# Optimization experiments

Measured on AMD Instinct MI355X. Metric: run time of the kernel, lower is better.

## Reference

```python
import jax, jax.numpy as jnp
import numpy as np


def _procrustes_align(X, Y):
    """Batched similarity-transform (scipy-style Procrustes, reflection allowed).
    Aligns Y (pred) to X (target). X, Y: [B, N, 3]. Returns aligned Y: [B, N, 3].
    """
    muX = X.mean(axis=1, keepdims=True)                      # [B,1,3]
    muY = Y.mean(axis=1, keepdims=True)
    X0 = X - muX
    Y0 = Y - muY
    normX = jnp.sqrt((X0 ** 2).sum(axis=(1, 2), keepdims=True))  # [B,1,1]
    normY = jnp.sqrt((Y0 ** 2).sum(axis=(1, 2), keepdims=True))
    X0n = X0 / normX
    Y0n = Y0 / normY
    # 3x3 cross-covariance per batch element
    M = jnp.einsum('bni,bnj->bij', X0n, Y0n)                 # [B,3,3]
    U, s, Vt = jnp.linalg.svd(M)                             # batched tiny SVD
    # Optimal rotation Q = V @ U^T = (U @ Vt)^T  (minimizes ||Y0n @ Q - X0n||)
    Q = jnp.swapaxes(jnp.matmul(U, Vt), -1, -2)              # [B,3,3]
    traceTA = s.sum(-1)[:, None, None]                       # [B,1,1]
    Z = normX * traceTA * jnp.einsum('bni,bij->bnj', Y0n, Q) + muX
    return Z


def setup_inputs() -> dict:
    key = jax.random.key(0)
    k1, k2 = jax.random.split(key)
    B, N = 262144, 21
    pred_kp3d = jax.random.normal(k1, (B, N, 3), dtype=jnp.float32)
    target_kp3d = jax.random.normal(k2, (B, N, 3), dtype=jnp.float32)
    return {"pred_kp3d": pred_kp3d, "target_kp3d": target_kp3d}


def reference(pred_kp3d, target_kp3d):
    pred_aligned = _procrustes_align(target_kp3d, pred_kp3d)
    # mean per-joint Euclidean distance (PA-MPJPE style)
    err = jnp.sqrt(((pred_aligned - target_kp3d) ** 2).sum(-1)).mean()
    return err
```

## Files before the change

### kernel.cpp

```cpp
#include <hip/hip_runtime.h>
#include <math.h>

#define NPTS 21
#define FLB  63
#define BPW  32
#define THREADS 64
#define TVEC (BPW * FLB / 4)
#define FULLR (TVEC / 64)
#define TAILL (TVEC % 64)
#define KMAX 11

__global__ __launch_bounds__(THREADS, 4)
void pa_mpjpe(const float* __restrict__ pred,
              const float* __restrict__ targ,
              float* __restrict__ ws,
              int B)
{
    __shared__ __align__(16) float ly[BPW * FLB];
    __shared__ __align__(16) float lx[BPW * FLB];

    const int lane = threadIdx.x & 63;
    const int b    = lane & (BPW - 1);
    const int sub  = (lane >> 5) & 1;
    const int b0   = blockIdx.x * BPW;

    const float4* gp = (const float4*)(pred + (size_t)b0 * FLB);
    const float4* gt = (const float4*)(targ + (size_t)b0 * FLB);
    float4 rp[FULLR + 1], rt[FULLR + 1];
    #pragma unroll
    for (int j = 0; j < FULLR; ++j) rp[j] = gp[j * 64 + lane];
    if (lane < TAILL)               rp[FULLR] = gp[FULLR * 64 + lane];
    #pragma unroll
    for (int j = 0; j < FULLR; ++j) rt[j] = gt[j * 64 + lane];
    if (lane < TAILL)               rt[FULLR] = gt[FULLR * 64 + lane];

    {
        float4* wy = (float4*)ly;
        float4* wx = (float4*)lx;
        #pragma unroll
        for (int j = 0; j < FULLR; ++j) wy[j * 64 + lane] = rp[j];
        if (lane < TAILL)               wy[FULLR * 64 + lane] = rp[FULLR];
        #pragma unroll
        for (int j = 0; j < FULLR; ++j) wx[j * 64 + lane] = rt[j];
        if (lane < TAILL)               wx[FULLR * 64 + lane] = rt[FULLR];
    }

    float py0[KMAX], py1[KMAX], py2[KMAX];
    float sy0=0.f, sy1=0.f, sy2=0.f, syy=0.f;
    float sx0=0.f, sx1=0.f, sx2=0.f;
    float m00=0,m01=0,m02=0, m10=0,m11=0,m12=0, m20=0,m21=0,m22=0;
    const int base = b * FLB;
    #pragma unroll
    for (int k = 0; k < KMAX; ++k) {
        const int n = 2 * k + sub;
        if (n < NPTS) {
            const int o = base + 3 * n;
            float a = ly[o+0], e = ly[o+1], c = ly[o+2];
            float u = lx[o+0], v = lx[o+1], x2 = lx[o+2];
            py0[k] = a; py1[k] = e; py2[k] = c;
            sy0 += a; sy1 += e; sy2 += c;
            syy = fmaf(a, a, fmaf(e, e, fmaf(c, c, syy)));
            sx0 += u; sx1 += v; sx2 += x2;
            m00 = fmaf(u,a,m00); m01 = fmaf(u,e,m01); m02 = fmaf(u,c,m02);
            m10 = fmaf(v,a,m10); m11 = fmaf(v,e,m11); m12 = fmaf(v,c,m12);
            m20 = fmaf(x2,a,m20); m21 = fmaf(x2,e,m21); m22 = fmaf(x2,c,m22);
        } else {
            py0[k] = 0.f; py1[k] = 0.f; py2[k] = 0.f;
        }
    }

    #define COMB(v) { v += __shfl_xor(v, 32, 64); }
    COMB(sy0) COMB(sy1) COMB(sy2) COMB(syy)
    COMB(sx0) COMB(sx1) COMB(sx2)
    COMB(m00) COMB(m01) COMB(m02)
    COMB(m10) COMB(m11) COMB(m12)
    COMB(m20) COMB(m21) COMB(m22)
    #undef COMB

    const float invN = 1.0f / (float)NPTS;
    float mux0 = sx0*invN, mux1 = sx1*invN, mux2 = sx2*invN;
    float muy0 = sy0*invN, muy1 = sy1*invN, muy2 = sy2*invN;
    float ny2  = syy - (sy0*sy0 + sy1*sy1 + sy2*sy2) * invN;
    float c00 = m00 - sx0*sy0*invN, c01 = m01 - sx0*sy1*invN, c02 = m02 - sx0*sy2*invN;
    float c10 = m10 - sx1*sy0*invN, c11 = m11 - sx1*sy1*invN, c12 = m12 - sx1*sy2*invN;
    float c20 = m20 - sx2*sy0*invN, c21 = m21 - sx2*sy1*invN, c22 = m22 - sx2*sy2*invN;

    float q00=c00, q01=c10, q02=c20,
          q10=c01, q11=c11, q12=c21,
          q20=c02, q21=c12, q22=c22;
    #pragma unroll
    for (int it = 0; it < 6; ++it) {
        float C00 = q11*q22 - q12*q21;
        float C01 = q12*q20 - q10*q22;
        float C02 = q10*q21 - q11*q20;
        float C10 = q02*q21 - q01*q22;
        float C11 = q00*q22 - q02*q20;
        float C12 = q01*q20 - q00*q21;
        float C20 = q01*q12 - q02*q11;
        float C21 = q02*q10 - q00*q12;
        float C22 = q00*q11 - q01*q10;
        float det = q00*C00 + q01*C01 + q02*C02;
        float ad  = fmaxf(fabsf(det), 1e-30f);
        float sdet = copysignf(ad, det);
        float g  = __expf(0.333333333f * __logf(ad));
        float ha = 0.5f / g;
        float hb = 0.5f * g / sdet;
        q00 = ha*q00 + hb*C00; q01 = ha*q01 + hb*C01; q02 = ha*q02 + hb*C02;
        q10 = ha*q10 + hb*C10; q11 = ha*q11 + hb*C11; q12 = ha*q12 + hb*C12;
        q20 = ha*q20 + hb*C20; q21 = ha*q21 + hb*C21; q22 = ha*q22 + hb*C22;
    }

    float trP = q00*c00 + q01*c10 + q02*c20
              + q10*c01 + q11*c11 + q12*c21
              + q20*c02 + q21*c12 + q22*c22;
    float kk = trP / ny2;
    float r00=kk*q00, r01=kk*q01, r02=kk*q02;
    float r10=kk*q10, r11=kk*q11, r12=kk*q12;
    float r20=kk*q20, r21=kk*q21, r22=kk*q22;

    float errsum = 0.0f;
    #pragma unroll
    for (int k = 0; k < KMAX; ++k) {
        const int n = 2 * k + sub;
        if (n < NPTS) {
            const int o = base + 3 * n;
            float xa = lx[o+0], xb = lx[o+1], xc = lx[o+2];
            float u = py0[k] - muy0, v = py1[k] - muy1, x2 = py2[k] - muy2;
            float z0 = fmaf(u, r00, fmaf(v, r10, fmaf(x2, r20, mux0))) - xa;
            float z1 = fmaf(u, r01, fmaf(v, r11, fmaf(x2, r21, mux1))) - xb;
            float z2 = fmaf(u, r02, fmaf(v, r12, fmaf(x2, r22, mux2))) - xc;
            errsum += sqrtf(fmaf(z0, z0, fmaf(z1, z1, z2*z2)));
        }
    }

    #pragma unroll
    for (int off = 32; off > 0; off >>= 1) errsum += __shfl_down(errsum, off, 64);
    if (lane == 0) ws[blockIdx.x] = errsum;
}

__global__ __launch_bounds__(256)
void pa_reduce(const float* __restrict__ ws, float* __restrict__ out,
               int nblk, float inv_total)
{
    __shared__ float sw[4];
    float s = 0.0f;
    const float4* w4 = (const float4*)ws;
    const int n4 = nblk >> 2;
    for (int i = threadIdx.x; i < n4; i += 256) {
        float4 v = w4[i];
        s += (v.x + v.y) + (v.z + v.w);
    }
    #pragma unroll
    for (int off = 32; off > 0; off >>= 1) s += __shfl_down(s, off, 64);
    if ((threadIdx.x & 63) == 0) sw[threadIdx.x >> 6] = s;
    __syncthreads();
    if (threadIdx.x == 0)
        out[0] = (sw[0] + sw[1] + sw[2] + sw[3]) * inv_total;
}

extern "C" void kernel_launch(void* const* d_in, const int* in_sizes, int n_in,
                              void* d_out, int out_size, void* d_ws, size_t ws_size,
                              hipStream_t stream)
{
    const float* pred = (const float*)d_in[0];
    const float* targ = (const float*)d_in[1];
    float* out = (float*)d_out;
    float* ws  = (float*)d_ws;

    int B = in_sizes[0] / FLB;
    int grid = (B + BPW - 1) / BPW;
    float inv_total = 1.0f / ((float)B * (float)NPTS);

    pa_mpjpe<<<grid, THREADS, 0, stream>>>(pred, targ, ws, B);
    pa_reduce<<<1, 256, 0, stream>>>(ws, out, grid, inv_total);
}
```

Measured before the change: 156.9 us.

## Process two batch chunks per block with a single reused LDS buffer and prefetch

Each 64-thread block now handles two 32-element chunks instead of one. A single LDS buffer is reused for pred then target, and the next chunk's global loads are issued while the current chunk is computed. Scheduling barriers fix the order so loads overlap compute. The goal is to hide global memory latency and halve LDS use per block, at the cost of more registers (occupancy hint lowered from 4 to 3) and half as many blocks.

```diff
diff --git a/kernel.cpp b/kernel.cpp
--- a/kernel.cpp
+++ b/kernel.cpp
@@ -3,135 +3,156 @@
 
 #define NPTS 21
 #define FLB  63
-#define BPW  32
+#define CB   32
+#define BPW  (2 * CB)
 #define THREADS 64
-#define TVEC (BPW * FLB / 4)
-#define FULLR (TVEC / 64)
-#define TAILL (TVEC % 64)
+#define TVEC (CB * FLB / 4)
+#define TAILL 56
 #define KMAX 11
 
-__global__ __launch_bounds__(THREADS, 4)
+#define SBAR() __builtin_amdgcn_sched_barrier(0)
+
+#define LOAD8(v, g) do { \
+    v##0 = (g)[0*64+lane]; v##1 = (g)[1*64+lane]; v##2 = (g)[2*64+lane]; \
+    v##3 = (g)[3*64+lane]; v##4 = (g)[4*64+lane]; v##5 = (g)[5*64+lane]; \
+    v##6 = (g)[6*64+lane]; if (lane < TAILL) v##7 = (g)[7*64+lane]; } while(0)
+
+#define STORE8(v) do { \
+    w4[0*64+lane] = v##0; w4[1*64+lane] = v##1; w4[2*64+lane] = v##2; \
+    w4[3*64+lane] = v##3; w4[4*64+lane] = v##4; w4[5*64+lane] = v##5; \
+    w4[6*64+lane] = v##6; if (lane < TAILL) w4[7*64+lane] = v##7; } while(0)
+
+#define PASSA() do { \
+    sy0=0.f; sy1=0.f; sy2=0.f; syy=0.f; \
+    _Pragma("unroll") \
+    for (int k = 0; k < KMAX; ++k) { \
+        const int n = 2*k + sub; \
+        if (n < NPTS) { \
+            const int o = base + 3*n; \
+            float a = sb[o+0], e = sb[o+1], c = sb[o+2]; \
+            py0[k]=a; py1[k]=e; py2[k]=c; \
+            sy0+=a; sy1+=e; sy2+=c; \
+            syy = fmaf(a,a,fmaf(e,e,fmaf(c,c,syy))); \
+        } else { py0[k]=0.f; py1[k]=0.f; py2[k]=0.f; } \
+    } } while(0)
+
+#define COMB(v) { v += __shfl_xor(v, 32, 64); }
+
+#define PASSB() do { \
+    float sx0=0.f, sx1=0.f, sx2=0.f; \
+    float m00=0,m01=0,m02=0, m10=0,m11=0,m12=0, m20=0,m21=0,m22=0; \
+    _Pragma("unroll") \
+    for (int k = 0; k < KMAX; ++k) { \
+        const int n = 2*k + sub; \
+        if (n < NPTS) { \
+            const int o = base + 3*n; \
+            float u = sb[o+0], v = sb[o+1], x2 = sb[o+2]; \
+            float a = py0[k], e = py1[k], c = py2[k]; \
+            sx0+=u; sx1+=v; sx2+=x2; \
+            m00=fmaf(u,a,m00); m01=fmaf(u,e,m01); m02=fmaf(u,c,m02); \
+            m10=fmaf(v,a,m10); m11=fmaf(v,e,m11); m12=fmaf(v,c,m12); \
+            m20=fmaf(x2,a,m20); m21=fmaf(x2,e,m21); m22=fmaf(x2,c,m22); \
+        } \
+    } \
+    COMB(sy0) COMB(sy1) COMB(sy2) COMB(syy) \
+    COMB(sx0) COMB(sx1) COMB(sx2) \
+    COMB(m00) COMB(m01) COMB(m02) \
+    COMB(m10) COMB(m11) COMB(m12) \
+    COMB(m20) COMB(m21) COMB(m22) \
+    const float invN = 1.0f / (float)NPTS; \
+    float mux0=sx0*invN, mux1=sx1*invN, mux2=sx2*invN; \
+    float muy0=sy0*invN, muy1=sy1*invN, muy2=sy2*invN; \
+    float ny2 = syy - (sy0*sy0 + sy1*sy1 + sy2*sy2) * invN; \
+    float c00=m00-sx0*sy0*invN, c01=m01-sx0*sy1*invN, c02=m02-sx0*sy2*invN; \
+    float c10=m10-sx1*sy0*invN, c11=m11-sx1*sy1*invN, c12=m12-sx1*sy2*invN; \
+    float c20=m20-sx2*sy0*invN, c21=m21-sx2*sy1*invN, c22=m22-sx2*sy2*invN; \
+    float q00=c00, q01=c10, q02=c20, \
+          q10=c01, q11=c11, q12=c21, \
+          q20=c02, q21=c12, q22=c22; \
+    _Pragma("unroll") \
+    for (int it = 0; it < 6; ++it) { \
+        float C00=q11*q22-q12*q21, C01=q12*q20-q10*q22, C02=q10*q21-q11*q20; \
+        float C10=q02*q21-q01*q22, C11=q00*q22-q02*q20, C12=q01*q20-q00*q21; \
+        float C20=q01*q12-q02*q11, C21=q02*q10-q00*q12, C22=q00*q11-q01*q10; \
+        float det = q00*C00 + q01*C01 + q02*C02; \
+        float ad  = fmaxf(fabsf(det), 1e-30f); \
+        float sdet = copysignf(ad, det); \
+        float g  = __expf(0.333333333f * __logf(ad)); \
+        float ha = 0.5f / g; \
+        float hb = 0.5f * g / sdet; \
+        q00=ha*q00+hb*C00; q01=ha*q01+hb*C01; q02=ha*q02+hb*C02; \
+        q10=ha*q10+hb*C10; q11=ha*q11+hb*C11; q12=ha*q12+hb*C12; \
+        q20=ha*q20+hb*C20; q21=ha*q21+hb*C21; q22=ha*q22+hb*C22; \
+    } \
+    float trP = q00*c00 + q01*c10 + q02*c20 \
+              + q10*c01 + q11*c11 + q12*c21 \
+              + q20*c02 + q21*c12 + q22*c22; \
+    float kk = trP / ny2; \
+    float r00=kk*q00, r01=kk*q01, r02=kk*q02; \
+    float r10=kk*q10, r11=kk*q11, r12=kk*q12; \
+    float r20=kk*q20, r21=kk*q21, r22=kk*q22; \
+    _Pragma("unroll") \
+    for (int k = 0; k < KMAX; ++k) { \
+        const int n = 2*k + sub; \
+        if (n < NPTS) { \
+            const int o = base + 3*n; \
+            float xa = sb[o+0], xb = sb[o+1], xc = sb[o+2]; \
+            float u = py0[k]-muy0, v = py1[k]-muy1, x2 = py2[k]-muy2; \
+            float z0 = fmaf(u,r00,fmaf(v,r10,fmaf(x2,r20,mux0))) - xa; \
+            float z1 = fmaf(u,r01,fmaf(v,r11,fmaf(x2,r21,mux1))) - xb; \
+            float z2 = fmaf(u,r02,fmaf(v,r12,fmaf(x2,r22,mux2))) - xc; \
+            errsum += sqrtf(fmaf(z0,z0,fmaf(z1,z1,z2*z2))); \
+        } \
+    } } while(0)
+
+__global__ __launch_bounds__(THREADS, 3)
 void pa_mpjpe(const float* __restrict__ pred,
               const float* __restrict__ targ,
               float* __restrict__ ws,
               int B)
 {
-    __shared__ __align__(16) float ly[BPW * FLB];
-    __shared__ __align__(16) float lx[BPW * FLB];
+    __shared__ __align__(16) float sb[CB * FLB];
+    float4* w4 = (float4*)sb;
 
     const int lane = threadIdx.x & 63;
-    const int b    = lane & (BPW - 1);
+    const int b    = lane & (CB - 1);
     const int sub  = (lane >> 5) & 1;
+    const int base = b * FLB;
     const int b0   = blockIdx.x * BPW;
 
-    const float4* gp = (const float4*)(pred + (size_t)b0 * FLB);
-    const float4* gt = (const float4*)(targ + (size_t)b0 * FLB);
-    float4 rp[FULLR + 1], rt[FULLR + 1];
-    #pragma unroll
-    for (int j = 0; j < FULLR; ++j) rp[j] = gp[j * 64 + lane];
-    if (lane < TAILL)               rp[FULLR] = gp[FULLR * 64 + lane];
-    #pragma unroll
-    for (int j = 0; j < FULLR; ++j) rt[j] = gt[j * 64 + lane];
-    if (lane < TAILL)               rt[FULLR] = gt[FULLR * 64 + lane];
+    const float4* gp0 = (const float4*)(pred + (size_t)b0 * FLB);
+    const float4* gt0 = (const float4*)(targ + (size_t)b0 * FLB);
+    const float4* gp1 = gp0 + TVEC;
+    const float4* gt1 = gt0 + TVEC;
 
-    {
-        float4* wy = (float4*)ly;
-        float4* wx = (float4*)lx;
-        #pragma unroll
-        for (int j = 0; j < FULLR; ++j) wy[j * 64 + lane] = rp[j];
-        if (lane < TAILL)               wy[FULLR * 64 + lane] = rp[FULLR];
-        #pragma unroll
-        for (int j = 0; j < FULLR; ++j) wx[j * 64 + lane] = rt[j];
-        if (lane < TAILL)               wx[FULLR * 64 + lane] = rt[FULLR];
-    }
+    float4 rp0, rp1, rp2, rp3, rp4, rp5, rp6, rp7 = make_float4(0,0,0,0);
+    float4 rt0, rt1, rt2, rt3, rt4, rt5, rt6, rt7 = make_float4(0,0,0,0);
+    float py0[KMAX], py1[KMAX], py2[KMAX];
+    float sy0, sy1, sy2, syy;
+    float errsum = 0.0f;
 
-    float py0[KMAX], py1[KMAX], py2[KMAX];
-    float sy0=0.f, sy1=0.f, sy2=0.f, syy=0.f;
-    float sx0=0.f, sx1=0.f, sx2=0.f;
-    float m00=0,m01=0,m02=0, m10=0,m11=0,m12=0, m20=0,m21=0,m22=0;
-    const int base = b * FLB;
-    #pragma unroll
-    for (int k = 0; k < KMAX; ++k) {
-        const int n = 2 * k + sub;
-        if (n < NPTS) {
-            const int o = base + 3 * n;
-            float a = ly[o+0], e = ly[o+1], c = ly[o+2];
-            float u = lx[o+0], v = lx[o+1], x2 = lx[o+2];
-            py0[k] = a; py1[k] = e; py2[k] = c;
-            sy0 += a; sy1 += e; sy2 += c;
-            syy = fmaf(a, a, fmaf(e, e, fmaf(c, c, syy)));
-            sx0 += u; sx1 += v; sx2 += x2;
-            m00 = fmaf(u,a,m00); m01 = fmaf(u,e,m01); m02 = fmaf(u,c,m02);
-            m10 = fmaf(v,a,m10); m11 = fmaf(v,e,m11); m12 = fmaf(v,c,m12);
-            m20 = fmaf(x2,a,m20); m21 = fmaf(x2,e,m21); m22 = fmaf(x2,c,m22);
-        } else {
-            py0[k] = 0.f; py1[k] = 0.f; py2[k] = 0.f;
-        }
-    }
-
-    #define COMB(v) { v += __shfl_xor(v, 32, 64); }
-    COMB(sy0) COMB(sy1) COMB(sy2) COMB(syy)
-    COMB(sx0) COMB(sx1) COMB(sx2)
-    COMB(m00) COMB(m01) COMB(m02)
-    COMB(m10) COMB(m11) COMB(m12)
-    COMB(m20) COMB(m21) COMB(m22)
-    #undef COMB
-
-    const float invN = 1.0f / (float)NPTS;
-    float mux0 = sx0*invN, mux1 = sx1*invN, mux2 = sx2*invN;
-    float muy0 = sy0*invN, muy1 = sy1*invN, muy2 = sy2*invN;
-    float ny2  = syy - (sy0*sy0 + sy1*sy1 + sy2*sy2) * invN;
-    float c00 = m00 - sx0*sy0*invN, c01 = m01 - sx0*sy1*invN, c02 = m02 - sx0*sy2*invN;
-    float c10 = m10 - sx1*sy0*invN, c11 = m11 - sx1*sy1*invN, c12 = m12 - sx1*sy2*invN;
-    float c20 = m20 - sx2*sy0*invN, c21 = m21 - sx2*sy1*invN, c22 = m22 - sx2*sy2*invN;
-
-    float q00=c00, q01=c10, q02=c20,
-          q10=c01, q11=c11, q12=c21,
-          q20=c02, q21=c12, q22=c22;
-    #pragma unroll
-    for (int it = 0; it < 6; ++it) {
-        float C00 = q11*q22 - q12*q21;
-        float C01 = q12*q20 - q10*q22;
-        float C02 = q10*q21 - q11*q20;
-        float C10 = q02*q21 - q01*q22;
-        float C11 = q00*q22 - q02*q20;
-        float C12 = q01*q20 - q00*q21;
-        float C20 = q01*q12 - q02*q11;
-        float C21 = q02*q10 - q00*q12;
-        float C22 = q00*q11 - q01*q10;
-        float det = q00*C00 + q01*C01 + q02*C02;
-        float ad  = fmaxf(fabsf(det), 1e-30f);
-        float sdet = copysignf(ad, det);
-        float g  = __expf(0.333333333f * __logf(ad));
-        float ha = 0.5f / g;
-        float hb = 0.5f * g / sdet;
-        q00 = ha*q00 + hb*C00; q01 = ha*q01 + hb*C01; q02 = ha*q02 + hb*C02;
-        q10 = ha*q10 + hb*C10; q11 = ha*q11 + hb*C11; q12 = ha*q12 + hb*C12;
-        q20 = ha*q20 + hb*C20; q21 = ha*q21 + hb*C21; q22 = ha*q22 + hb*C22;
-    }
-
-    float trP = q00*c00 + q01*c10 + q02*c20
-              + q10*c01 + q11*c11 + q12*c21
-              + q20*c02 + q21*c12 + q22*c22;
-    float kk = trP / ny2;
-    float r00=kk*q00, r01=kk*q01, r02=kk*q02;
-    float r10=kk*q10, r11=kk*q11, r12=kk*q12;
-    float r20=kk*q20, r21=kk*q21, r22=kk*q22;
-
-    float errsum = 0.0f;
-    #pragma unroll
-    for (int k = 0; k < KMAX; ++k) {
-        const int n = 2 * k + sub;
-        if (n < NPTS) {
-            const int o = base + 3 * n;
-            float xa = lx[o+0], xb = lx[o+1], xc = lx[o+2];
-            float u = py0[k] - muy0, v = py1[k] - muy1, x2 = py2[k] - muy2;
-            float z0 = fmaf(u, r00, fmaf(v, r10, fmaf(x2, r20, mux0))) - xa;
-            float z1 = fmaf(u, r01, fmaf(v, r11, fmaf(x2, r21, mux1))) - xb;
-            float z2 = fmaf(u, r02, fmaf(v, r12, fmaf(x2, r22, mux2))) - xc;
-            errsum += sqrtf(fmaf(z0, z0, fmaf(z1, z1, z2*z2)));
-        }
-    }
+    LOAD8(rp, gp0);
+    LOAD8(rt, gt0);
+    SBAR();
+    STORE8(rp);
+    SBAR();
+    LOAD8(rp, gp1);
+    SBAR();
+    PASSA();
+    SBAR();
+    STORE8(rt);
+    SBAR();
+    LOAD8(rt, gt1);
+    SBAR();
+    PASSB();
+    SBAR();
+    STORE8(rp);
+    SBAR();
+    PASSA();
+    SBAR();
+    STORE8(rt);
+    SBAR();
+    PASSB();
 
     #pragma unroll
     for (int off = 32; off > 0; off >>= 1) errsum += __shfl_down(errsum, off, 64);
```

Result: no change. 154.7 us (-1.4%).
